# Kernel optimization log

Measured on AMD Instinct MI355X. Metric: run time of the kernel, lower is better.

The kernel has to match this reference:

```python
import jax, jax.numpy as jnp
import numpy as np

DIM = 768
NUM_HEADS = 12
MLP_RATIO = 4.0
HIDDEN = int(DIM * MLP_RATIO)
EPS = 1e-6  # flax LayerNorm default


def setup_inputs() -> dict:
    key = jax.random.key(0)
    ks = jax.random.split(key, 8)
    d = DIM
    init = lambda k, shape, fan_in: jax.random.normal(k, shape, jnp.float32) * (fan_in ** -0.5)
    return {
        "x": jax.random.normal(ks[0], (8, 1024, d), jnp.float32),
        "ln1_scale": jnp.ones((d,), jnp.float32),
        "ln1_bias": jnp.zeros((d,), jnp.float32),
        "qkv_w": init(ks[1], (d, 3 * d), d),
        "qkv_b": jnp.zeros((3 * d,), jnp.float32),
        "proj_w": init(ks[2], (d, d), d),
        "proj_b": jnp.zeros((d,), jnp.float32),
        "ln2_scale": jnp.ones((d,), jnp.float32),
        "ln2_bias": jnp.zeros((d,), jnp.float32),
        "fc1_w": init(ks[3], (d, HIDDEN), d),
        "fc1_b": jnp.zeros((HIDDEN,), jnp.float32),
        "fc2_w": init(ks[4], (HIDDEN, d), HIDDEN),
        "fc2_b": jnp.zeros((d,), jnp.float32),
    }


def _layernorm(x, scale, bias):
    mu = jnp.mean(x, axis=-1, keepdims=True)
    var = jnp.mean(jnp.square(x - mu), axis=-1, keepdims=True)
    return (x - mu) * jax.lax.rsqrt(var + EPS) * scale + bias


def reference(x, ln1_scale, ln1_bias, qkv_w, qkv_b, proj_w, proj_b,
              ln2_scale, ln2_bias, fc1_w, fc1_b, fc2_w, fc2_b):
    b, n, d = x.shape
    h = NUM_HEADS
    hd = d // h
    scale = hd ** -0.5

    # --- attention (pre-norm) ---
    y = _layernorm(x, ln1_scale, ln1_bias)
    qkv = y @ qkv_w + qkv_b                      # [b, n, 3d]
    qkv = qkv.reshape(b, n, 3, h, hd).transpose(2, 0, 3, 1, 4)  # [3, b, h, n, hd]
    q, k, v = qkv[0], qkv[1], qkv[2]
    attn = jnp.einsum("bhqd,bhkd->bhqk", q, k) * scale
    attn = jax.nn.softmax(attn, axis=-1)
    o = jnp.einsum("bhqk,bhkd->bhqd", attn, v)   # [b, h, n, hd]
    o = o.transpose(0, 2, 1, 3).reshape(b, n, d)
    x = x + (o @ proj_w + proj_b)

    # --- MLP (pre-norm) ---
    y = _layernorm(x, ln2_scale, ln2_bias)
    y = jax.nn.gelu(y @ fc1_w + fc1_b)
    x = x + (y @ fc2_w + fc2_b)
    return x
```

## Files before the change

kernel.cpp:

```cpp
#include <hip/hip_runtime.h>
#include <hip/hip_bf16.h>
#include <math.h>


#define DIM 768
#define SEQ 1024
#define BATCH 8
#define NHEAD 12
#define HDIM 64
#define HID 3072
#define MTOK (BATCH * SEQ)

typedef __attribute__((ext_vector_type(8))) short short8;
typedef __attribute__((ext_vector_type(4))) short short4v;
typedef __attribute__((ext_vector_type(4))) float floatx4;

__device__ __forceinline__ short f2s(float x) {
  __hip_bfloat16 h = __float2bfloat16(x);
  return __builtin_bit_cast(short, h);
}
__device__ __forceinline__ float s2f(short s) {
  return __bfloat162float(__builtin_bit_cast(__hip_bfloat16, s));
}
__device__ __forceinline__ floatx4 zf4() {
  floatx4 v; v[0] = v[1] = v[2] = v[3] = 0.f; return v;
}
__device__ __forceinline__ float gelu_f(float x) {
  float z = 0.7978845608028654f * (x + 0.044715f * x * x * x);
  float u = __expf(2.f * z);
  return 0.5f * x * (2.f - 2.f / (u + 1.f));
}

__global__ __launch_bounds__(256) void tr_kernel(const float* __restrict__ in,
                                                 short* __restrict__ out, int K, int N) {
  __shared__ float tile[32][33];
  const int tx = threadIdx.x, ty = threadIdx.y;
  const int n0 = blockIdx.x * 32, k0 = blockIdx.y * 32;
#pragma unroll
  for (int i = 0; i < 4; ++i)
    tile[ty + i * 8][tx] = in[(size_t)(k0 + ty + i * 8) * N + n0 + tx];
  __syncthreads();
#pragma unroll
  for (int i = 0; i < 4; ++i)
    out[(size_t)(n0 + ty + i * 8) * K + k0 + tx] = f2s(tile[tx][ty + i * 8]);
}

__global__ __launch_bounds__(256) void ln_kernel(const float* __restrict__ x,
                                                 const float* __restrict__ scale,
                                                 const float* __restrict__ bias,
                                                 short* __restrict__ y) {
  const int row = blockIdx.x;
  const int t = threadIdx.x;
  const float* xr = x + (size_t)row * DIM;
  float v[3];
  float s1 = 0.f, s2 = 0.f;
#pragma unroll
  for (int j = 0; j < 3; ++j) {
    v[j] = xr[t + j * 256];
    s1 += v[j];
    s2 += v[j] * v[j];
  }
#pragma unroll
  for (int off = 32; off; off >>= 1) {
    s1 += __shfl_down(s1, off, 64);
    s2 += __shfl_down(s2, off, 64);
  }
  __shared__ float r1[4], r2[4], bc[2];
  const int wave = t >> 6, lane = t & 63;
  if (lane == 0) { r1[wave] = s1; r2[wave] = s2; }
  __syncthreads();
  if (t == 0) {
    float S1 = r1[0] + r1[1] + r1[2] + r1[3];
    float S2 = r2[0] + r2[1] + r2[2] + r2[3];
    float mu = S1 * (1.0f / DIM);
    float var = S2 * (1.0f / DIM) - mu * mu;
    bc[0] = mu;
    bc[1] = rsqrtf(fmaxf(var, 0.f) + 1e-6f);
  }
  __syncthreads();
  const float mu = bc[0], rstd = bc[1];
#pragma unroll
  for (int j = 0; j < 3; ++j) {
    const int idx = t + j * 256;
    y[(size_t)row * DIM + idx] = f2s((v[j] - mu) * rstd * scale[idx] + bias[idx]);
  }
}

__device__ __forceinline__ void stage_tile(const short* __restrict__ src, int ld,
                                           short* lds, int t) {
  const int lane = t & 63;
  const int w = t >> 6;
#pragma unroll
  for (int i = 0; i < 2; ++i) {
    const int S = w * 128 + i * 64 + lane;
    const int row = S >> 2;
    const int chunk = (S & 3) ^ ((row >> 1) & 3);
    const short* g = src + (size_t)row * ld + chunk * 8;
    const unsigned off = __builtin_amdgcn_readfirstlane((unsigned)((w * 128 + i * 64) * 16));
    __builtin_amdgcn_global_load_lds(
        (const __attribute__((address_space(1))) void*)g,
        (__attribute__((address_space(3))) void*)((char*)lds + off), 16, 0, 0);
  }
}

template <int MODE>
__global__ __launch_bounds__(256) void gemm_mfma(
    const short* __restrict__ A, const short* __restrict__ Bt,
    const float* __restrict__ bias, const float* __restrict__ res,
    float* __restrict__ outF, short* __restrict__ outB,
    short* __restrict__ Qb, short* __restrict__ Kb, short* __restrict__ Vtb,
    int N, int K) {
  __shared__ __align__(16) short Asm[4096];
  __shared__ __align__(16) short Bsm[4096];
  const int t = threadIdx.x;
  const int lane = t & 63, w = t >> 6, quad = lane >> 4, l15 = lane & 15;
  const int m0 = blockIdx.y * 128, n0 = blockIdx.x * 128;
  const int mb = (w & 1) * 64, nb = (w >> 1) * 64;

  floatx4 acc[4][4];
#pragma unroll
  for (int mi = 0; mi < 4; ++mi)
#pragma unroll
    for (int ni = 0; ni < 4; ++ni) acc[mi][ni] = zf4();

  for (int kt = 0; kt < K; kt += 32) {
    __syncthreads();
    stage_tile(A + (size_t)m0 * K + kt, K, Asm, t);
    stage_tile(Bt + (size_t)n0 * K + kt, K, Bsm, t);
    __syncthreads();
    short8 a[4], b[4];
#pragma unroll
    for (int mi = 0; mi < 4; ++mi) {
      const int r = mb + mi * 16 + l15;
      a[mi] = *(const short8*)(Asm + r * 32 + (quad ^ ((r >> 1) & 3)) * 8);
    }
#pragma unroll
    for (int ni = 0; ni < 4; ++ni) {
      const int r = nb + ni * 16 + l15;
      b[ni] = *(const short8*)(Bsm + r * 32 + (quad ^ ((r >> 1) & 3)) * 8);
    }
#pragma unroll
    for (int mi = 0; mi < 4; ++mi)
#pragma unroll
      for (int ni = 0; ni < 4; ++ni)
        acc[mi][ni] = __builtin_amdgcn_mfma_f32_16x16x32_bf16(a[mi], b[ni], acc[mi][ni], 0, 0, 0);
  }

#pragma unroll
  for (int mi = 0; mi < 4; ++mi) {
    const int row0 = m0 + mb + mi * 16 + quad * 4;
#pragma unroll
    for (int ni = 0; ni < 4; ++ni) {
      const int col = n0 + nb + ni * 16 + l15;
      const float bv = bias[col];
      float v[4];
#pragma unroll
      for (int r = 0; r < 4; ++r) v[r] = acc[mi][ni][r] + bv;
      if (MODE == 0) {
        const int bb = row0 >> 10;
        const int s0 = row0 & 1023;
        if (col < 1536) {
          const int cc = (col < 768) ? col : col - 768;
          const int h = cc >> 6, d = cc & 63;
          short* dst = (col < 768 ? Qb : Kb) + (size_t)(bb * NHEAD + h) * SEQ * HDIM;
#pragma unroll
          for (int r = 0; r < 4; ++r) dst[(size_t)(s0 + r) * HDIM + d] = f2s(v[r]);
        } else {
          const int cc = col - 1536;
          const int h = cc >> 6, d = cc & 63;
          short4v pv;
#pragma unroll
          for (int r = 0; r < 4; ++r) pv[r] = f2s(v[r]);
          *(short4v*)(Vtb + ((size_t)(bb * NHEAD + h) * HDIM + d) * SEQ + s0) = pv;
        }
      } else if (MODE == 1) {
#pragma unroll
        for (int r = 0; r < 4; ++r) {
          const size_t idx = (size_t)(row0 + r) * N + col;
          outF[idx] = v[r] + res[idx];
        }
      } else {
#pragma unroll
        for (int r = 0; r < 4; ++r)
          outB[(size_t)(row0 + r) * N + col] = f2s(gelu_f(v[r]));
      }
    }
  }
}

__device__ __forceinline__ void stage64(const short* __restrict__ src, int ld,
                                        short* lds, int t) {
  const int lane = t & 63, w = t >> 6;
#pragma unroll
  for (int i = 0; i < 2; ++i) {
    const int S = w * 128 + i * 64 + lane;
    const int r = S >> 3, c0 = S & 7;
    const int c = c0 ^ (r & 7);
    const short* g = src + (size_t)r * ld + c * 8;
    const unsigned off = __builtin_amdgcn_readfirstlane((unsigned)((w * 128 + i * 64) * 16));
    __builtin_amdgcn_global_load_lds(
        (const __attribute__((address_space(1))) void*)g,
        (__attribute__((address_space(3))) void*)((char*)lds + off), 16, 0, 0);
  }
}

__global__ __launch_bounds__(256) void attn_kernel(
    const short* __restrict__ Qb, const short* __restrict__ Kb,
    const short* __restrict__ Vtb, short* __restrict__ o) {
  __shared__ __align__(16) short Ks[2][4096];
  __shared__ __align__(16) short Vts[2][4096];
  __shared__ __align__(16) short Pt[8192];
  const int t = threadIdx.x;
  const int lane = t & 63, w = t >> 6, quad = lane >> 4, l15 = lane & 15;
  const int q0 = blockIdx.x * 128;
  const int bh = blockIdx.y;
  const size_t qkbase = (size_t)bh * SEQ * HDIM;
  const size_t vbase = (size_t)bh * HDIM * SEQ;
  short* ptw = Pt + w * 2048;

  short8 bq[2][2];
#pragma unroll
  for (int mi = 0; mi < 2; ++mi)
#pragma unroll
    for (int ks = 0; ks < 2; ++ks)
      bq[mi][ks] = *(const short8*)(Qb + qkbase +
                                    (size_t)(q0 + w * 32 + mi * 16 + l15) * HDIM +
                                    ks * 32 + quad * 8);

  floatx4 oacc[4][2];
  float m_st[2], l_st[2];
#pragma unroll
  for (int mi = 0; mi < 2; ++mi) { m_st[mi] = -1e30f; l_st[mi] = 0.f; }
#pragma unroll
  for (int di = 0; di < 4; ++di)
#pragma unroll
    for (int mi = 0; mi < 2; ++mi) oacc[di][mi] = zf4();

  stage64(Kb + qkbase, HDIM, Ks[0], t);
  stage64(Vtb + vbase, SEQ, Vts[0], t);

  for (int kt = 0; kt < 16; ++kt) {
    __syncthreads();
    const int cur = kt & 1;
    if (kt < 15) {
      stage64(Kb + qkbase + (size_t)(kt + 1) * 64 * HDIM, HDIM, Ks[cur ^ 1], t);
      stage64(Vtb + vbase + (kt + 1) * 64, SEQ, Vts[cur ^ 1], t);
    }

    floatx4 sacc[4][2];
#pragma unroll
    for (int ni = 0; ni < 4; ++ni)
#pragma unroll
      for (int mi = 0; mi < 2; ++mi) sacc[ni][mi] = zf4();
#pragma unroll
    for (int ks = 0; ks < 2; ++ks) {
      short8 ak[4];
#pragma unroll
      for (int ni = 0; ni < 4; ++ni) {
        const int r = ni * 16 + l15;
        ak[ni] = *(const short8*)(Ks[cur] + r * 64 + (((ks * 4 + quad) ^ (r & 7)) * 8));
      }
#pragma unroll
      for (int ni = 0; ni < 4; ++ni)
#pragma unroll
        for (int mi = 0; mi < 2; ++mi)
          sacc[ni][mi] = __builtin_amdgcn_mfma_f32_16x16x32_bf16(ak[ni], bq[mi][ks], sacc[ni][mi], 0, 0, 0);
    }

    float alpha[2];
#pragma unroll
    for (int mi = 0; mi < 2; ++mi) {
      float mx = -1e30f;
#pragma unroll
      for (int ni = 0; ni < 4; ++ni)
#pragma unroll
        for (int r = 0; r < 4; ++r) mx = fmaxf(mx, sacc[ni][mi][r]);
      mx = fmaxf(mx, __shfl_xor(mx, 16, 64));
      mx = fmaxf(mx, __shfl_xor(mx, 32, 64));
      mx *= 0.125f;
      const float mn = fmaxf(m_st[mi], mx);
      alpha[mi] = __expf(m_st[mi] - mn);
      m_st[mi] = mn;
      float rs = 0.f;
      const int row = mi * 16 + l15;
      const int swz = (row & 7) ^ ((row & 8) >> 1);
#pragma unroll
      for (int ni = 0; ni < 4; ++ni) {
        short4v pk;
#pragma unroll
        for (int r = 0; r < 4; ++r) {
          const float p = __expf(sacc[ni][mi][r] * 0.125f - mn);
          rs += p;
          pk[r] = f2s(p);
        }
        const int c = ni * 2 + (quad >> 1);
        *(short4v*)(ptw + row * 64 + ((c ^ swz) * 8 + (quad & 1) * 4)) = pk;
      }
      rs += __shfl_xor(rs, 16, 64);
      rs += __shfl_xor(rs, 32, 64);
      l_st[mi] = l_st[mi] * alpha[mi] + rs;
    }
#pragma unroll
    for (int di = 0; di < 4; ++di)
#pragma unroll
      for (int mi = 0; mi < 2; ++mi)
#pragma unroll
        for (int r = 0; r < 4; ++r) oacc[di][mi][r] *= alpha[mi];

#pragma unroll
    for (int ks = 0; ks < 2; ++ks) {
      short8 bp[2];
#pragma unroll
      for (int mi = 0; mi < 2; ++mi) {
        const int row = mi * 16 + l15;
        const int swz = (row & 7) ^ ((row & 8) >> 1);
        bp[mi] = *(const short8*)(ptw + row * 64 + (((ks * 4 + quad) ^ swz) * 8));
      }
      short8 av[4];
#pragma unroll
      for (int di = 0; di < 4; ++di) {
        const int r = di * 16 + l15;
        av[di] = *(const short8*)(Vts[cur] + r * 64 + (((ks * 4 + quad) ^ (r & 7)) * 8));
      }
#pragma unroll
      for (int di = 0; di < 4; ++di)
#pragma unroll
        for (int mi = 0; mi < 2; ++mi)
          oacc[di][mi] = __builtin_amdgcn_mfma_f32_16x16x32_bf16(av[di], bp[mi], oacc[di][mi], 0, 0, 0);
    }
  }

  const int bb = bh / NHEAD, hh = bh % NHEAD;
  float inv[2];
#pragma unroll
  for (int mi = 0; mi < 2; ++mi) inv[mi] = 1.0f / l_st[mi];
#pragma unroll
  for (int di = 0; di < 4; ++di)
#pragma unroll
    for (int mi = 0; mi < 2; ++mi) {
      const int tok = bb * SEQ + q0 + w * 32 + mi * 16 + l15;
      const int d = hh * HDIM + di * 16 + quad * 4;
      short4v ov;
#pragma unroll
      for (int r = 0; r < 4; ++r) ov[r] = f2s(oacc[di][mi][r] * inv[mi]);
      *(short4v*)(o + (size_t)tok * DIM + d) = ov;
    }
}

extern "C" void kernel_launch(void* const* d_in, const int* in_sizes, int n_in,
                              void* d_out, int out_size, void* d_ws, size_t ws_size,
                              hipStream_t stream) {
  const float* x      = (const float*)d_in[0];
  const float* ln1_s  = (const float*)d_in[1];
  const float* ln1_b  = (const float*)d_in[2];
  const float* qkv_w  = (const float*)d_in[3];
  const float* qkv_b  = (const float*)d_in[4];
  const float* proj_w = (const float*)d_in[5];
  const float* proj_b = (const float*)d_in[6];
  const float* ln2_s  = (const float*)d_in[7];
  const float* ln2_b  = (const float*)d_in[8];
  const float* fc1_w  = (const float*)d_in[9];
  const float* fc1_b  = (const float*)d_in[10];
  const float* fc2_w  = (const float*)d_in[11];
  const float* fc2_b  = (const float*)d_in[12];
  float* out = (float*)d_out;

  char* p = (char*)d_ws;
  short* wqt = (short*)p; p += (size_t)(3 * DIM) * DIM * 2;
  short* wpt = (short*)p; p += (size_t)DIM * DIM * 2;
  short* w1t = (short*)p; p += (size_t)HID * DIM * 2;
  short* w2t = (short*)p; p += (size_t)DIM * HID * 2;
  short* y   = (short*)p; p += (size_t)MTOK * DIM * 2;
  short* Qb  = (short*)p; p += (size_t)MTOK * DIM * 2;
  short* Kb  = (short*)p; p += (size_t)MTOK * DIM * 2;
  short* Vtb = (short*)p; p += (size_t)MTOK * DIM * 2;
  float* x1  = (float*)p; p += (size_t)MTOK * DIM * 4;
  short* h   = (short*)p; p += (size_t)MTOK * HID * 2;
  short* obuf = y;
  short* y2   = Qb;

  tr_kernel<<<dim3((3 * DIM) / 32, DIM / 32), dim3(32, 8), 0, stream>>>(qkv_w, wqt, DIM, 3 * DIM);
  tr_kernel<<<dim3(DIM / 32, DIM / 32), dim3(32, 8), 0, stream>>>(proj_w, wpt, DIM, DIM);
  tr_kernel<<<dim3(HID / 32, DIM / 32), dim3(32, 8), 0, stream>>>(fc1_w, w1t, DIM, HID);
  tr_kernel<<<dim3(DIM / 32, HID / 32), dim3(32, 8), 0, stream>>>(fc2_w, w2t, HID, DIM);

  ln_kernel<<<MTOK, 256, 0, stream>>>(x, ln1_s, ln1_b, y);
  gemm_mfma<0><<<dim3((3 * DIM) / 128, MTOK / 128), 256, 0, stream>>>(
      y, wqt, qkv_b, nullptr, nullptr, nullptr, Qb, Kb, Vtb, 3 * DIM, DIM);
  attn_kernel<<<dim3(SEQ / 128, BATCH * NHEAD), 256, 0, stream>>>(Qb, Kb, Vtb, obuf);
  gemm_mfma<1><<<dim3(DIM / 128, MTOK / 128), 256, 0, stream>>>(
      obuf, wpt, proj_b, x, x1, nullptr, nullptr, nullptr, nullptr, DIM, DIM);
  ln_kernel<<<MTOK, 256, 0, stream>>>(x1, ln2_s, ln2_b, y2);
  gemm_mfma<2><<<dim3(HID / 128, MTOK / 128), 256, 0, stream>>>(
      y2, w1t, fc1_b, nullptr, nullptr, h, nullptr, nullptr, nullptr, HID, DIM);
  gemm_mfma<1><<<dim3(DIM / 128, MTOK / 128), 256, 0, stream>>>(
      h, w2t, fc2_b, x1, out, nullptr, nullptr, nullptr, nullptr, DIM, HID);
}
```

Baseline: 416.6 us.

## Double-buffer GEMM LDS staging, remap blocks per XCD, narrow N tiles, fuse transposes

The GEMM main loop now uses two LDS buffers and issues the global-to-LDS loads for the next K tile before computing on the current one. This drops one barrier per iteration and is meant to hide load latency. Block indices are remapped so that neighbouring M tiles go to the same XCD, which should improve L2 reuse. The proj and fc2 GEMMs (N=768) switch to 64-wide N tiles so more blocks run. The four weight-transpose launches are merged into one kernel. The risks are higher LDS use, which may lower occupancy, and a possible read/write race on the buffer being refilled, since only one barrier per iteration remains.

```diff
diff --git a/kernel.cpp b/kernel.cpp
--- a/kernel.cpp
+++ b/kernel.cpp
@@ -31,11 +31,23 @@
   return 0.5f * x * (2.f - 2.f / (u + 1.f));
 }
 
-__global__ __launch_bounds__(256) void tr_kernel(const float* __restrict__ in,
-                                                 short* __restrict__ out, int K, int N) {
+__global__ __launch_bounds__(256) void tr4_kernel(
+    const float* __restrict__ w0, short* __restrict__ o0,
+    const float* __restrict__ w1, short* __restrict__ o1,
+    const float* __restrict__ w2, short* __restrict__ o2,
+    const float* __restrict__ w3, short* __restrict__ o3) {
   __shared__ float tile[32][33];
-  const int tx = threadIdx.x, ty = threadIdx.y;
-  const int n0 = blockIdx.x * 32, k0 = blockIdx.y * 32;
+  const int id = blockIdx.x;
+  const float* in;
+  short* out;
+  int K, N, tid;
+  if (id < 1728)      { in = w0; out = o0; K = DIM; N = 3 * DIM; tid = id; }
+  else if (id < 2304) { in = w1; out = o1; K = DIM; N = DIM;     tid = id - 1728; }
+  else if (id < 4608) { in = w2; out = o2; K = DIM; N = HID;     tid = id - 2304; }
+  else                { in = w3; out = o3; K = HID; N = DIM;     tid = id - 4608; }
+  const int ntx = N >> 5;
+  const int n0 = (tid % ntx) * 32, k0 = (tid / ntx) * 32;
+  const int tx = threadIdx.x & 31, ty = threadIdx.x >> 5;
 #pragma unroll
   for (int i = 0; i < 4; ++i)
     tile[ty + i * 8][tx] = in[(size_t)(k0 + ty + i * 8) * N + n0 + tx];
@@ -86,63 +98,76 @@
   }
 }
 
-__device__ __forceinline__ void stage_tile(const short* __restrict__ src, int ld,
-                                           short* lds, int t) {
-  const int lane = t & 63;
-  const int w = t >> 6;
-#pragma unroll
-  for (int i = 0; i < 2; ++i) {
-    const int S = w * 128 + i * 64 + lane;
+template <int ROWS>
+__device__ __forceinline__ void stage(const short* __restrict__ src, int ld,
+                                      short* lds, int t) {
+  const int lane = t & 63, w = t >> 6;
+  constexpr int ITER = ROWS / 64;
+#pragma unroll
+  for (int i = 0; i < ITER; ++i) {
+    const int S = w * (64 * ITER) + i * 64 + lane;
     const int row = S >> 2;
     const int chunk = (S & 3) ^ ((row >> 1) & 3);
     const short* g = src + (size_t)row * ld + chunk * 8;
-    const unsigned off = __builtin_amdgcn_readfirstlane((unsigned)((w * 128 + i * 64) * 16));
+    const unsigned off = __builtin_amdgcn_readfirstlane((unsigned)((w * (64 * ITER) + i * 64) * 16));
     __builtin_amdgcn_global_load_lds(
         (const __attribute__((address_space(1))) void*)g,
         (__attribute__((address_space(3))) void*)((char*)lds + off), 16, 0, 0);
   }
 }
 
-template <int MODE>
+template <int MODE, int NT>
 __global__ __launch_bounds__(256) void gemm_mfma(
     const short* __restrict__ A, const short* __restrict__ Bt,
     const float* __restrict__ bias, const float* __restrict__ res,
     float* __restrict__ outF, short* __restrict__ outB,
     short* __restrict__ Qb, short* __restrict__ Kb, short* __restrict__ Vtb,
     int N, int K) {
-  __shared__ __align__(16) short Asm[4096];
-  __shared__ __align__(16) short Bsm[4096];
+  constexpr int NI = NT / 32;
+  __shared__ __align__(16) short Asm[2][4096];
+  __shared__ __align__(16) short Bsm[2][NT * 32];
   const int t = threadIdx.x;
   const int lane = t & 63, w = t >> 6, quad = lane >> 4, l15 = lane & 15;
-  const int m0 = blockIdx.y * 128, n0 = blockIdx.x * 128;
-  const int mb = (w & 1) * 64, nb = (w >> 1) * 64;
-
-  floatx4 acc[4][4];
+
+  const int nbx = gridDim.x;
+  const int lid = blockIdx.y * nbx + blockIdx.x;
+  const int xcd = lid & 7, local = lid >> 3;
+  const int m0 = ((local / nbx) * 8 + xcd) * 128;
+  const int n0 = (local % nbx) * NT;
+  const int mb = (w & 1) * 64, nb = (w >> 1) * (NT / 2);
+
+  floatx4 acc[4][NI];
 #pragma unroll
   for (int mi = 0; mi < 4; ++mi)
 #pragma unroll
-    for (int ni = 0; ni < 4; ++ni) acc[mi][ni] = zf4();
-
-  for (int kt = 0; kt < K; kt += 32) {
+    for (int ni = 0; ni < NI; ++ni) acc[mi][ni] = zf4();
+
+  stage<128>(A + (size_t)m0 * K, K, Asm[0], t);
+  stage<NT>(Bt + (size_t)n0 * K, K, Bsm[0], t);
+
+  const int nk = K >> 5;
+  for (int kt = 0; kt < nk; ++kt) {
     __syncthreads();
-    stage_tile(A + (size_t)m0 * K + kt, K, Asm, t);
-    stage_tile(Bt + (size_t)n0 * K + kt, K, Bsm, t);
-    __syncthreads();
-    short8 a[4], b[4];
+    const int cur = kt & 1;
+    if (kt + 1 < nk) {
+      stage<128>(A + (size_t)m0 * K + (kt + 1) * 32, K, Asm[cur ^ 1], t);
+      stage<NT>(Bt + (size_t)n0 * K + (kt + 1) * 32, K, Bsm[cur ^ 1], t);
+    }
+    short8 a[4], b[NI];
 #pragma unroll
     for (int mi = 0; mi < 4; ++mi) {
       const int r = mb + mi * 16 + l15;
-      a[mi] = *(const short8*)(Asm + r * 32 + (quad ^ ((r >> 1) & 3)) * 8);
-    }
-#pragma unroll
-    for (int ni = 0; ni < 4; ++ni) {
+      a[mi] = *(const short8*)(Asm[cur] + r * 32 + (quad ^ ((r >> 1) & 3)) * 8);
+    }
+#pragma unroll
+    for (int ni = 0; ni < NI; ++ni) {
       const int r = nb + ni * 16 + l15;
-      b[ni] = *(const short8*)(Bsm + r * 32 + (quad ^ ((r >> 1) & 3)) * 8);
+      b[ni] = *(const short8*)(Bsm[cur] + r * 32 + (quad ^ ((r >> 1) & 3)) * 8);
     }
 #pragma unroll
     for (int mi = 0; mi < 4; ++mi)
 #pragma unroll
-      for (int ni = 0; ni < 4; ++ni)
+      for (int ni = 0; ni < NI; ++ni)
         acc[mi][ni] = __builtin_amdgcn_mfma_f32_16x16x32_bf16(a[mi], b[ni], acc[mi][ni], 0, 0, 0);
   }
 
@@ -150,7 +175,7 @@
   for (int mi = 0; mi < 4; ++mi) {
     const int row0 = m0 + mb + mi * 16 + quad * 4;
 #pragma unroll
-    for (int ni = 0; ni < 4; ++ni) {
+    for (int ni = 0; ni < NI; ++ni) {
       const int col = n0 + nb + ni * 16 + l15;
       const float bv = bias[col];
       float v[4];
@@ -379,20 +404,17 @@
   short* obuf = y;
   short* y2   = Qb;
 
-  tr_kernel<<<dim3((3 * DIM) / 32, DIM / 32), dim3(32, 8), 0, stream>>>(qkv_w, wqt, DIM, 3 * DIM);
-  tr_kernel<<<dim3(DIM / 32, DIM / 32), dim3(32, 8), 0, stream>>>(proj_w, wpt, DIM, DIM);
-  tr_kernel<<<dim3(HID / 32, DIM / 32), dim3(32, 8), 0, stream>>>(fc1_w, w1t, DIM, HID);
-  tr_kernel<<<dim3(DIM / 32, HID / 32), dim3(32, 8), 0, stream>>>(fc2_w, w2t, HID, DIM);
+  tr4_kernel<<<6912, 256, 0, stream>>>(qkv_w, wqt, proj_w, wpt, fc1_w, w1t, fc2_w, w2t);
 
   ln_kernel<<<MTOK, 256, 0, stream>>>(x, ln1_s, ln1_b, y);
-  gemm_mfma<0><<<dim3((3 * DIM) / 128, MTOK / 128), 256, 0, stream>>>(
+  gemm_mfma<0, 128><<<dim3(18, 64), 256, 0, stream>>>(
       y, wqt, qkv_b, nullptr, nullptr, nullptr, Qb, Kb, Vtb, 3 * DIM, DIM);
   attn_kernel<<<dim3(SEQ / 128, BATCH * NHEAD), 256, 0, stream>>>(Qb, Kb, Vtb, obuf);
-  gemm_mfma<1><<<dim3(DIM / 128, MTOK / 128), 256, 0, stream>>>(
+  gemm_mfma<1, 64><<<dim3(12, 64), 256, 0, stream>>>(
       obuf, wpt, proj_b, x, x1, nullptr, nullptr, nullptr, nullptr, DIM, DIM);
   ln_kernel<<<MTOK, 256, 0, stream>>>(x1, ln2_s, ln2_b, y2);
-  gemm_mfma<2><<<dim3(HID / 128, MTOK / 128), 256, 0, stream>>>(
+  gemm_mfma<2, 128><<<dim3(24, 64), 256, 0, stream>>>(
       y2, w1t, fc1_b, nullptr, nullptr, h, nullptr, nullptr, nullptr, HID, DIM);
-  gemm_mfma<1><<<dim3(DIM / 128, MTOK / 128), 256, 0, stream>>>(
+  gemm_mfma<1, 64><<<dim3(12, 64), 256, 0, stream>>>(
       h, w2t, fc2_b, x1, out, nullptr, nullptr, nullptr, nullptr, DIM, HID);
 }
```

After: 395.8 us. 5.0% less time.
